# Optimization experiments

Measured on AMD Instinct MI355X. Metric: run time of the kernel, lower is better.

Reference implementation:

```python
import jax, jax.numpy as jnp
import numpy as np

N_NODES = 50000
N_EDGES = 800000
IN_DIM = 128
OUT_DIM = 64
K_KERNELS = 2
S_ATTEN = 2


def setup_inputs() -> dict:
    key = jax.random.key(0)
    ks = jax.random.split(key, 9)
    return {
        "x": jax.random.normal(ks[0], (N_NODES, IN_DIM), dtype=jnp.float32),
        "support_vals": jax.random.uniform(ks[1], (K_KERNELS, N_EDGES), dtype=jnp.float32),
        "atten_vals": jax.random.uniform(ks[2], (S_ATTEN, N_EDGES), dtype=jnp.float32),
        "W_transform": jax.random.normal(ks[3], (K_KERNELS, IN_DIM, OUT_DIM), dtype=jnp.float32) * 0.05,
        "w_left": jax.random.normal(ks[4], (K_KERNELS, S_ATTEN + 1, OUT_DIM), dtype=jnp.float32) * 0.05,
        "w_right": jax.random.normal(ks[5], (K_KERNELS, S_ATTEN + 1, OUT_DIM), dtype=jnp.float32) * 0.05,
        "W_residual": jax.random.normal(ks[6], (IN_DIM + OUT_DIM, OUT_DIM), dtype=jnp.float32) * 0.05,
        "edge_rows": jax.random.randint(ks[7], (N_EDGES,), 0, N_NODES, dtype=jnp.int64),
        "edge_cols": jax.random.randint(ks[8], (N_EDGES,), 0, N_NODES, dtype=jnp.int64),
    }


def reference(x, support_vals, atten_vals, W_transform, w_left, w_right, W_residual, edge_rows, edge_cols):
    # x: [N, F], edge lists: [E]; all supports share the same sparsity pattern.
    N = x.shape[0]
    K = W_transform.shape[0]
    output = jnp.zeros((N, W_transform.shape[2]), dtype=x.dtype)
    for k in range(K):
        wx = x @ W_transform[k]                       # [N, D]
        al = wx @ w_left[k].T                         # [N, S+1]
        ar = wx @ w_right[k].T                        # [N, S+1]
        # per-support edge values; support i=S uses this kernel's Cheb support
        vals = jnp.concatenate([atten_vals, support_vals[k][None, :]], axis=0)  # [S+1, E]
        # score_e = sum_i (al[row_e,i] + ar[col_e,i]) * vals[i,e]
        scores = jnp.einsum('es,se->e', al[edge_rows] + ar[edge_cols], vals)    # [E]
        # row-wise (segment) softmax over nonzeros, as tf.sparse_softmax
        m = jax.ops.segment_max(scores, edge_rows, num_segments=N)              # [N]
        ex = jnp.exp(scores - m[edge_rows])
        denom = jax.ops.segment_sum(ex, edge_rows, num_segments=N)              # [N]
        probs = ex / denom[edge_rows]                                           # [E]
        # spmm: out[r] = sum_{e: row_e=r} probs_e * wx[col_e]
        output = output + jax.ops.segment_sum(probs[:, None] * wx[edge_cols], edge_rows, num_segments=N)
    # residual projection then elu activation
    output = jnp.concatenate([x, output], axis=-1) @ W_residual
    return jax.nn.elu(output)
```

## Files before the change

### kernel.cpp

```cpp
#include <hip/hip_runtime.h>

#define N_NODES 50000
#define N_EDGES 800000
#define IN_DIM 128
#define OUT_DIM 64
#define NEG_INF (-1e30f)
#define GBLK ((N_NODES + 63) / 64)
#define BSHIFT 7
#define NBUK ((N_NODES + 127) >> 7)
#define NBUKP 392
#define EB 1024
#define PREB ((N_EDGES + EB - 1) / EB)
#define NFRAG (3 * 16 + 8)
#define STAGE_CAP 3072

typedef unsigned short ushort_t;
typedef __attribute__((ext_vector_type(8))) short short8;
typedef __attribute__((ext_vector_type(4))) float f32x4;

__device__ __forceinline__ unsigned f2bf(float f) {
    unsigned u = __float_as_uint(f);
    u += 0x7fffu + ((u >> 16) & 1u);
    return u >> 16;
}
__device__ __forceinline__ unsigned rl_u(unsigned v, int i) {
    return __builtin_amdgcn_readlane(v, i);
}
__device__ __forceinline__ float rl_f(float v, int i) {
    return __uint_as_float(__builtin_amdgcn_readlane(__float_as_uint(v), i));
}

__global__ void wpack_kernel(const float* __restrict__ Wt,
                             const float* __restrict__ Wres,
                             ushort_t* __restrict__ Wpack) {
    int idx = blockIdx.x * 256 + threadIdx.x;
    if (idx >= NFRAG * 512) return;
    int f = idx >> 9;
    int within = idx & 511;
    int lane = within >> 3;
    int b = within & 7;
    float val;
    if (f < 48) {
        int mat = f >> 4;
        int ct = (f >> 2) & 3;
        int kc = f & 3;
        int k = kc * 32 + (lane >> 4) * 8 + b;
        int c = ct * 16 + (lane & 15);
        const float* W = (mat < 2) ? (Wt + (size_t)mat * IN_DIM * OUT_DIM) : Wres;
        val = W[(size_t)k * OUT_DIM + c];
    } else {
        int f2 = f - 48;
        int ct = f2 >> 1;
        int kc = f2 & 1;
        int k = kc * 32 + (lane >> 4) * 8 + b;
        int c = ct * 16 + (lane & 15);
        val = Wres[(size_t)(IN_DIM + k) * OUT_DIM + c];
    }
    Wpack[idx] = (ushort_t)f2bf(val);
}

__global__ __launch_bounds__(256) void gemm_kernel(
        const float* __restrict__ x,
        const ushort_t* __restrict__ Wpack,
        const float* __restrict__ wl,
        const float* __restrict__ wr,
        unsigned* __restrict__ wxi,
        float* __restrict__ xres,
        float* __restrict__ al,
        float* __restrict__ ar) {
    int wave = threadIdx.x >> 6;
    int lane = threadIdx.x & 63;
    int lr = lane & 15;
    int lg = lane >> 4;
    int row0 = blockIdx.x * 64 + wave * 16;

    int arow = row0 + lr;
    if (arow >= N_NODES) arow = N_NODES - 1;
    const float* xr = x + (size_t)arow * IN_DIM;
    short8 afrag[4];
#pragma unroll
    for (int kc = 0; kc < 4; ++kc) {
        float4 f0 = *(const float4*)(xr + kc * 32 + lg * 8);
        float4 f1 = *(const float4*)(xr + kc * 32 + lg * 8 + 4);
        short8 a;
        a[0] = (short)f2bf(f0.x); a[1] = (short)f2bf(f0.y);
        a[2] = (short)f2bf(f0.z); a[3] = (short)f2bf(f0.w);
        a[4] = (short)f2bf(f1.x); a[5] = (short)f2bf(f1.y);
        a[6] = (short)f2bf(f1.z); a[7] = (short)f2bf(f1.w);
        afrag[kc] = a;
    }

    f32x4 acc[3][4] = {};
#pragma unroll
    for (int kc = 0; kc < 4; ++kc) {
#pragma unroll
        for (int mat = 0; mat < 3; ++mat) {
#pragma unroll
            for (int ct = 0; ct < 4; ++ct) {
                short8 bfrag = *(const short8*)(
                    Wpack + (size_t)(((mat * 4 + ct) * 4 + kc) << 9) + lane * 8);
                acc[mat][ct] = __builtin_amdgcn_mfma_f32_16x16x32_bf16(
                    afrag[kc], bfrag, acc[mat][ct], 0, 0, 0);
            }
        }
    }

#pragma unroll
    for (int r = 0; r < 4; ++r) {
        int gr = row0 + lg * 4 + r;
        if (gr < N_NODES) {
#pragma unroll
            for (int ct = 0; ct < 4; ++ct) {
                unsigned pk = f2bf(acc[0][ct][r]) | (f2bf(acc[1][ct][r]) << 16);
                wxi[(size_t)gr * OUT_DIM + ct * 16 + lr] = pk;
                xres[(size_t)gr * OUT_DIM + ct * 16 + lr] = acc[2][ct][r];
            }
        }
    }

#pragma unroll
    for (int mat = 0; mat < 2; ++mat) {
#pragma unroll
        for (int s = 0; s < 3; ++s) {
            float wlv[4], wrv[4];
#pragma unroll
            for (int ct = 0; ct < 4; ++ct) {
                wlv[ct] = wl[(size_t)(mat * 3 + s) * OUT_DIM + ct * 16 + lr];
                wrv[ct] = wr[(size_t)(mat * 3 + s) * OUT_DIM + ct * 16 + lr];
            }
#pragma unroll
            for (int r = 0; r < 4; ++r) {
                float pl = 0.f, pr = 0.f;
#pragma unroll
                for (int ct = 0; ct < 4; ++ct) {
                    pl = fmaf(acc[mat][ct][r], wlv[ct], pl);
                    pr = fmaf(acc[mat][ct][r], wrv[ct], pr);
                }
#pragma unroll
                for (int off = 1; off < 16; off <<= 1) {
                    pl += __shfl_xor(pl, off);
                    pr += __shfl_xor(pr, off);
                }
                if (lr == 0) {
                    int gr = row0 + lg * 4 + r;
                    if (gr < N_NODES) {
                        al[(size_t)gr * 6 + mat * 3 + s] = pl;
                        ar[(size_t)gr * 6 + mat * 3 + s] = pr;
                    }
                }
            }
        }
    }
}

__global__ __launch_bounds__(256) void score_sort_kernel(
        const int* __restrict__ rows,
        const int* __restrict__ cols,
        const float* __restrict__ atten,
        const float* __restrict__ support,
        const float* __restrict__ al,
        const float* __restrict__ ar,
        uint4* __restrict__ etmp,
        uint2* __restrict__ cl) {
    __shared__ int cnt[512];
    __shared__ int cur[512];
    __shared__ int aux[256];
    __shared__ uint4 stage[EB];
    int t = threadIdx.x;
    cnt[t] = 0; cnt[t + 256] = 0;
    __syncthreads();
    int base0 = blockIdx.x * EB;
    int nval = min(EB, N_EDGES - base0);

    int r_[4], c_[4];
    float s0_[4], s1_[4];
#pragma unroll
    for (int i = 0; i < 4; ++i) {
        int e = base0 + i * 256 + t;
        bool v = e < N_EDGES;
        int r = v ? rows[e] : -1;
        int c = v ? cols[e] : 0;
        float sc0 = 0.f, sc1 = 0.f;
        if (v) {
            float a0 = atten[e], a1 = atten[N_EDGES + e];
            float sp0 = support[e], sp1 = support[N_EDGES + e];
            const float* A = al + (size_t)r * 6;
            const float* B = ar + (size_t)c * 6;
            sc0 = (A[0] + B[0]) * a0 + (A[1] + B[1]) * a1 + (A[2] + B[2]) * sp0;
            sc1 = (A[3] + B[3]) * a0 + (A[4] + B[4]) * a1 + (A[5] + B[5]) * sp1;
            atomicAdd(&cnt[r >> BSHIFT], 1);
        }
        r_[i] = r; c_[i] = c; s0_[i] = sc0; s1_[i] = sc1;
    }
    __syncthreads();
    int a0 = cnt[2 * t], a1 = cnt[2 * t + 1];
    int ps = a0 + a1;
    aux[t] = ps;
    __syncthreads();
    int val = ps;
    for (int off = 1; off < 256; off <<= 1) {
        int y = (t >= off) ? aux[t - off] : 0;
        __syncthreads();
        val += y; aux[t] = val;
        __syncthreads();
    }
    int e2 = val - ps;
    cur[2 * t] = e2;
    cur[2 * t + 1] = e2 + a0;
    size_t cb = (size_t)blockIdx.x * NBUKP;
    if (2 * t < NBUK)     cl[cb + 2 * t]     = make_uint2((unsigned)a0, (unsigned)e2);
    if (2 * t + 1 < NBUK) cl[cb + 2 * t + 1] = make_uint2((unsigned)a1, (unsigned)(e2 + a0));
    __syncthreads();
#pragma unroll
    for (int i = 0; i < 4; ++i) {
        if (r_[i] < 0) continue;
        int pos = atomicAdd(&cur[r_[i] >> BSHIFT], 1);
        uint4 pv;
        pv.x = (unsigned)c_[i] | ((unsigned)(r_[i] & 127) << 16);
        pv.y = __float_as_uint(s0_[i]);
        pv.z = __float_as_uint(s1_[i]);
        pv.w = 0u;
        stage[pos] = pv;
    }
    __syncthreads();
    for (int i = t; i < nval; i += 256)
        etmp[(size_t)base0 + i] = stage[i];
}

__global__ void colscan_kernel(const uint2* __restrict__ cl,
                               int* __restrict__ btot) {
    __shared__ int sh[256];
    int k = blockIdx.x, t = threadIdx.x;
    int s = 0;
    for (int b = t; b < PREB; b += 256) s += (int)cl[(size_t)b * NBUKP + k].x;
    sh[t] = s;
    __syncthreads();
    for (int off = 128; off > 0; off >>= 1) {
        if (t < off) sh[t] += sh[t + off];
        __syncthreads();
    }
    if (t == 0) btot[k] = sh[0];
}

__global__ __launch_bounds__(256) void sortb_kernel(
        const uint2* __restrict__ cl,
        const int* __restrict__ btot,
        const uint4* __restrict__ etmp,
        uint4* __restrict__ edata,
        int* __restrict__ row_ptr) {
    __shared__ uint4 stage[STAGE_CAP];
    __shared__ int rpos[PREB + 2];
    __shared__ int lloff[PREB];
    __shared__ int aux[256];
    __shared__ int bb[512];
    __shared__ int hist[128], rcur[128];
    int k = blockIdx.x, t = threadIdx.x;

    bb[t] = (t < NBUK) ? btot[t] : 0;
    bb[t + 256] = (t + 256 < NBUK) ? btot[t + 256] : 0;
    __syncthreads();
    int a0 = bb[2 * t], a1 = bb[2 * t + 1];
    int ps = a0 + a1;
    aux[t] = ps;
    __syncthreads();
    int val = ps;
    for (int off = 1; off < 256; off <<= 1) {
        int y = (t >= off) ? aux[t - off] : 0;
        __syncthreads();
        val += y; aux[t] = val;
        __syncthreads();
    }
    bb[2 * t] = val - ps;
    bb[2 * t + 1] = val - ps + a0;
    __syncthreads();
    int base = bb[k];

    for (int b = t; b < PREB; b += 256) {
        uint2 v2 = cl[(size_t)b * NBUKP + k];
        rpos[b] = (int)v2.x;
        lloff[b] = (int)v2.y;
    }
    if (t < 128) hist[t] = 0;
    __syncthreads();
    int v[4];
    int idx4 = 4 * t;
#pragma unroll
    for (int i = 0; i < 4; ++i) v[i] = (idx4 + i < PREB) ? rpos[idx4 + i] : 0;
    __syncthreads();
    int s = 0;
#pragma unroll
    for (int i = 0; i < 4; ++i) { int tmp = v[i]; v[i] = s; s += tmp; }
    aux[t] = s;
    __syncthreads();
    int tv = s;
    for (int off = 1; off < 256; off <<= 1) {
        int y = (t >= off) ? aux[t - off] : 0;
        __syncthreads();
        tv += y; aux[t] = tv;
        __syncthreads();
    }
    int ofs = tv - s;
#pragma unroll
    for (int i = 0; i < 4; ++i)
        if (idx4 + i <= PREB) rpos[idx4 + i] = ofs + v[i];
    __syncthreads();
    int nb = rpos[PREB];

    for (int b = t; b < PREB; b += 256) {
        int s0 = rpos[b];
        int n = rpos[b + 1] - s0;
        int lo = lloff[b];
        const uint4* src = etmp + (size_t)b * EB + lo;
        for (int i = 0; i < n; ++i) {
            uint4 rec = src[i];
            int j = s0 + i;
            if (j < STAGE_CAP) stage[j] = rec;
            atomicAdd(&hist[(rec.x >> 16) & 127], 1);
        }
    }
    __syncthreads();
    int hv = (t < 128) ? hist[t] : 0;
    aux[t] = hv;
    __syncthreads();
    int hval = hv;
    for (int off = 1; off < 128; off <<= 1) {
        int y = (t >= off && t < 128) ? aux[t - off] : 0;
        __syncthreads();
        hval += y; aux[t] = hval;
        __syncthreads();
    }
    if (t < 128) {
        rcur[t] = hval - hv;
        int row = (k << BSHIFT) + t;
        if (row < N_NODES) row_ptr[row] = base + hval - hv;
    }
    if (k == NBUK - 1 && t == 0) row_ptr[N_NODES] = N_EDGES;
    __syncthreads();
    for (int j = t; j < nb; j += 256) {
        uint4 rec;
        if (j < STAGE_CAP) rec = stage[j];
        else {
            int lo = 0, hi = PREB - 1;
            while (lo < hi) { int mid = (lo + hi + 1) >> 1; if (rpos[mid] <= j) lo = mid; else hi = mid - 1; }
            rec = etmp[(size_t)lo * EB + lloff[lo] + (j - rpos[lo])];
        }
        int rl = (rec.x >> 16) & 127;
        int dst = atomicAdd(&rcur[rl], 1);
        edata[(size_t)base + dst] = rec;
    }
}

__global__ void attn_kernel(const int* __restrict__ row_ptr,
                            const uint4* __restrict__ edata,
                            const unsigned* __restrict__ wxi,
                            ushort_t* __restrict__ aacc) {
    int wid = blockIdx.x * 4 + (threadIdx.x >> 6);
    if (wid >= N_NODES) return;
    int lane = threadIdx.x & 63;
    int beg = row_ptr[wid], end = row_ptr[wid + 1];
    int deg = end - beg;
    float a = 0.f;

    if (deg > 0 && deg <= 64) {
        bool valid = lane < deg;
        uint4 ed = edata[valid ? beg + lane : beg];
        unsigned c = ed.x & 0xFFFFu;
        float sc0 = valid ? __uint_as_float(ed.y) : NEG_INF;
        float sc1 = valid ? __uint_as_float(ed.z) : NEG_INF;
        float m0 = sc0, m1 = sc1;
#pragma unroll
        for (int off = 32; off > 0; off >>= 1) {
            m0 = fmaxf(m0, __shfl_xor(m0, off));
            m1 = fmaxf(m1, __shfl_xor(m1, off));
        }
        float e0 = valid ? __expf(sc0 - m0) : 0.f;
        float e1 = valid ? __expf(sc1 - m1) : 0.f;
        float l0 = e0, l1 = e1;
#pragma unroll
        for (int off = 32; off > 0; off >>= 1) {
            l0 += __shfl_xor(l0, off);
            l1 += __shfl_xor(l1, off);
        }
        float p0 = e0 / l0;
        float p1 = e1 / l1;
        float acc8[8] = {};
        int i = 0;
        for (; i + 8 <= deg; i += 8) {
            unsigned cc[8], vv[8];
#pragma unroll
            for (int j = 0; j < 8; ++j) cc[j] = rl_u(c, i + j);
#pragma unroll
            for (int j = 0; j < 8; ++j) vv[j] = wxi[(size_t)cc[j] * OUT_DIM + lane];
#pragma unroll
            for (int j = 0; j < 8; ++j) {
                acc8[j] = fmaf(rl_f(p0, i + j), __uint_as_float(vv[j] << 16), acc8[j]);
                acc8[j] = fmaf(rl_f(p1, i + j), __uint_as_float(vv[j] & 0xffff0000u), acc8[j]);
            }
        }
        for (; i < deg; ++i) {
            unsigned ci = rl_u(c, i);
            unsigned v = wxi[(size_t)ci * OUT_DIM + lane];
            acc8[0] = fmaf(rl_f(p0, i), __uint_as_float(v << 16), acc8[0]);
            acc8[0] = fmaf(rl_f(p1, i), __uint_as_float(v & 0xffff0000u), acc8[0]);
        }
        a = ((acc8[0] + acc8[1]) + (acc8[2] + acc8[3]))
          + ((acc8[4] + acc8[5]) + (acc8[6] + acc8[7]));
    } else if (deg > 64) {
        float m0 = NEG_INF, l0 = 0.f, m1 = NEG_INF, l1 = 0.f;
        for (int base = beg; base < end; base += 64) {
            int pos = base + lane;
            bool valid = pos < end;
            uint4 ed = edata[valid ? pos : beg];
            float sc0 = valid ? __uint_as_float(ed.y) : NEG_INF;
            float sc1 = valid ? __uint_as_float(ed.z) : NEG_INF;
            float cm0 = sc0, cm1 = sc1;
#pragma unroll
            for (int off = 32; off > 0; off >>= 1) {
                cm0 = fmaxf(cm0, __shfl_xor(cm0, off));
                cm1 = fmaxf(cm1, __shfl_xor(cm1, off));
            }
            float mn0 = fmaxf(m0, cm0), mn1 = fmaxf(m1, cm1);
            float e0 = valid ? __expf(sc0 - mn0) : 0.f;
            float e1 = valid ? __expf(sc1 - mn1) : 0.f;
#pragma unroll
            for (int off = 32; off > 0; off >>= 1) {
                e0 += __shfl_xor(e0, off);
                e1 += __shfl_xor(e1, off);
            }
            l0 = l0 * __expf(m0 - mn0) + e0;
            l1 = l1 * __expf(m1 - mn1) + e1;
            m0 = mn0; m1 = mn1;
        }
        float inv0 = 1.f / l0, inv1 = 1.f / l1;
        for (int base = beg; base < end; base += 64) {
            int pos = base + lane;
            bool valid = pos < end;
            uint4 ed = edata[valid ? pos : beg];
            unsigned c = ed.x & 0xFFFFu;
            float p0 = valid ? __expf(__uint_as_float(ed.y) - m0) * inv0 : 0.f;
            float p1 = valid ? __expf(__uint_as_float(ed.z) - m1) * inv1 : 0.f;
            int cnt = min(64, end - base);
            for (int i = 0; i < cnt; ++i) {
                unsigned ci = rl_u(c, i);
                unsigned v = wxi[(size_t)ci * OUT_DIM + lane];
                a = fmaf(rl_f(p0, i), __uint_as_float(v << 16), a);
                a = fmaf(rl_f(p1, i), __uint_as_float(v & 0xffff0000u), a);
            }
        }
    }
    aacc[(size_t)wid * OUT_DIM + lane] = (ushort_t)f2bf(a);
}

__global__ __launch_bounds__(256) void resid_kernel(
        const ushort_t* __restrict__ aacc,
        const float* __restrict__ xres,
        const ushort_t* __restrict__ Wpack,
        float* __restrict__ out) {
    int wave = threadIdx.x >> 6;
    int lane = threadIdx.x & 63;
    int lr = lane & 15;
    int lg = lane >> 4;
    int row0 = blockIdx.x * 64 + wave * 16;
    int arow = row0 + lr;
    if (arow >= N_NODES) arow = N_NODES - 1;
    const ushort_t* ap = aacc + (size_t)arow * OUT_DIM;
    short8 af[2];
#pragma unroll
    for (int kc = 0; kc < 2; ++kc)
        af[kc] = *(const short8*)(ap + kc * 32 + lg * 8);
    f32x4 acc4[4] = {};
#pragma unroll
    for (int kc = 0; kc < 2; ++kc) {
#pragma unroll
        for (int ct = 0; ct < 4; ++ct) {
            short8 bfrag = *(const short8*)(
                Wpack + (size_t)((48 + ct * 2 + kc) << 9) + lane * 8);
            acc4[ct] = __builtin_amdgcn_mfma_f32_16x16x32_bf16(
                af[kc], bfrag, acc4[ct], 0, 0, 0);
        }
    }
#pragma unroll
    for (int r = 0; r < 4; ++r) {
        int gr = row0 + lg * 4 + r;
        if (gr < N_NODES) {
#pragma unroll
            for (int ct = 0; ct < 4; ++ct) {
                float v = acc4[ct][r] + xres[(size_t)gr * OUT_DIM + ct * 16 + lr];
                out[(size_t)gr * OUT_DIM + ct * 16 + lr] = (v > 0.f) ? v : expm1f(v);
            }
        }
    }
}

extern "C" void kernel_launch(void* const* d_in, const int* in_sizes, int n_in,
                              void* d_out, int out_size, void* d_ws, size_t ws_size,
                              hipStream_t stream) {
    const float* x       = (const float*)d_in[0];
    const float* support = (const float*)d_in[1];
    const float* atten   = (const float*)d_in[2];
    const float* Wt      = (const float*)d_in[3];
    const float* wl      = (const float*)d_in[4];
    const float* wr      = (const float*)d_in[5];
    const float* Wres    = (const float*)d_in[6];
    const int*   rows    = (const int*)d_in[7];
    const int*   cols    = (const int*)d_in[8];
    float* out = (float*)d_out;

    unsigned* wxi   = (unsigned*)d_ws;
    float* xres     = (float*)(wxi + (size_t)N_NODES * OUT_DIM);
    float* al       = xres + (size_t)N_NODES * OUT_DIM;
    float* ar       = al + (size_t)N_NODES * 6;
    uint4* etmp     = (uint4*)(ar + (size_t)N_NODES * 6);
    uint4* edata    = etmp + (size_t)N_EDGES;
    int*   row_ptr  = (int*)(edata + (size_t)N_EDGES);
    uint2* cl       = (uint2*)(row_ptr + N_NODES + 4);
    int*   btot     = (int*)(cl + (size_t)PREB * NBUKP);
    ushort_t* Wpack = (ushort_t*)(btot + NBUK + 4);
    ushort_t* aacc  = (ushort_t*)etmp;

    wpack_kernel<<<(NFRAG * 512 + 255) / 256, 256, 0, stream>>>(Wt, Wres, Wpack);
    gemm_kernel<<<GBLK, 256, 0, stream>>>(x, Wpack, wl, wr, wxi, xres, al, ar);
    score_sort_kernel<<<PREB, 256, 0, stream>>>(
        rows, cols, atten, support, al, ar, etmp, cl);
    colscan_kernel<<<NBUK, 256, 0, stream>>>(cl, btot);
    sortb_kernel<<<NBUK, 256, 0, stream>>>(
        cl, btot, etmp, edata, row_ptr);
    attn_kernel<<<(N_NODES + 3) / 4, 256, 0, stream>>>(
        row_ptr, edata, wxi, aacc);
    resid_kernel<<<GBLK, 256, 0, stream>>>(aacc, xres, Wpack, out);
}
```

Baseline: 140.3 us.

## Use fp16 dot2 for SpMM accumulation and fold bucket totals into score kernel

Two changes. First, wx for the two kernels is stored as packed fp16 pairs instead of bf16, and the edge probabilities are packed as half2, so each neighbour accumulates with a single v_dot2 instruction instead of two FMAs plus unpacking. Second, the separate column-scan kernel that summed per-bucket counts is removed; score_sort now atomically adds its counts into btot, which is cleared by a memset beforehand. The intent is to cut ALU work in the attention loop and one kernel launch, at the cost of fp16 range and precision limits and global atomic contention.

```diff
diff --git a/kernel.cpp b/kernel.cpp
--- a/kernel.cpp
+++ b/kernel.cpp
@@ -17,6 +17,7 @@
 typedef unsigned short ushort_t;
 typedef __attribute__((ext_vector_type(8))) short short8;
 typedef __attribute__((ext_vector_type(4))) float f32x4;
+typedef __attribute__((ext_vector_type(2))) _Float16 half2_t;
 
 __device__ __forceinline__ unsigned f2bf(float f) {
     unsigned u = __float_as_uint(f);
@@ -28,6 +29,15 @@
 }
 __device__ __forceinline__ float rl_f(float v, int i) {
     return __uint_as_float(__builtin_amdgcn_readlane(__float_as_uint(v), i));
+}
+__device__ __forceinline__ unsigned pack_h2(float a, float b) {
+    auto h = __builtin_amdgcn_cvt_pkrtz(a, b);
+    union { decltype(h) h2; unsigned u; } v; v.h2 = h; return v.u;
+}
+__device__ __forceinline__ float dot2u(unsigned w, unsigned p, float acc) {
+    union { unsigned u; half2_t h; } wv, pv;
+    wv.u = w; pv.u = p;
+    return __builtin_amdgcn_fdot2(wv.h, pv.h, acc, false);
 }
 
 __global__ void wpack_kernel(const float* __restrict__ Wt,
@@ -111,8 +121,8 @@
         if (gr < N_NODES) {
 #pragma unroll
             for (int ct = 0; ct < 4; ++ct) {
-                unsigned pk = f2bf(acc[0][ct][r]) | (f2bf(acc[1][ct][r]) << 16);
-                wxi[(size_t)gr * OUT_DIM + ct * 16 + lr] = pk;
+                wxi[(size_t)gr * OUT_DIM + ct * 16 + lr] =
+                    pack_h2(acc[0][ct][r], acc[1][ct][r]);
                 xres[(size_t)gr * OUT_DIM + ct * 16 + lr] = acc[2][ct][r];
             }
         }
@@ -161,7 +171,8 @@
         const float* __restrict__ al,
         const float* __restrict__ ar,
         uint4* __restrict__ etmp,
-        uint2* __restrict__ cl) {
+        uint2* __restrict__ cl,
+        int* __restrict__ btot) {
     __shared__ int cnt[512];
     __shared__ int cur[512];
     __shared__ int aux[256];
@@ -208,8 +219,14 @@
     cur[2 * t] = e2;
     cur[2 * t + 1] = e2 + a0;
     size_t cb = (size_t)blockIdx.x * NBUKP;
-    if (2 * t < NBUK)     cl[cb + 2 * t]     = make_uint2((unsigned)a0, (unsigned)e2);
-    if (2 * t + 1 < NBUK) cl[cb + 2 * t + 1] = make_uint2((unsigned)a1, (unsigned)(e2 + a0));
+    if (2 * t < NBUK) {
+        cl[cb + 2 * t] = make_uint2((unsigned)a0, (unsigned)e2);
+        if (a0) atomicAdd(&btot[2 * t], a0);
+    }
+    if (2 * t + 1 < NBUK) {
+        cl[cb + 2 * t + 1] = make_uint2((unsigned)a1, (unsigned)(e2 + a0));
+        if (a1) atomicAdd(&btot[2 * t + 1], a1);
+    }
     __syncthreads();
 #pragma unroll
     for (int i = 0; i < 4; ++i) {
@@ -225,21 +242,6 @@
     __syncthreads();
     for (int i = t; i < nval; i += 256)
         etmp[(size_t)base0 + i] = stage[i];
-}
-
-__global__ void colscan_kernel(const uint2* __restrict__ cl,
-                               int* __restrict__ btot) {
-    __shared__ int sh[256];
-    int k = blockIdx.x, t = threadIdx.x;
-    int s = 0;
-    for (int b = t; b < PREB; b += 256) s += (int)cl[(size_t)b * NBUKP + k].x;
-    sh[t] = s;
-    __syncthreads();
-    for (int off = 128; off > 0; off >>= 1) {
-        if (t < off) sh[t] += sh[t + off];
-        __syncthreads();
-    }
-    if (t == 0) btot[k] = sh[0];
 }
 
 __global__ __launch_bounds__(256) void sortb_kernel(
@@ -381,8 +383,7 @@
             l0 += __shfl_xor(l0, off);
             l1 += __shfl_xor(l1, off);
         }
-        float p0 = e0 / l0;
-        float p1 = e1 / l1;
+        unsigned pp = pack_h2(e0 / l0, e1 / l1);
         float acc8[8] = {};
         int i = 0;
         for (; i + 8 <= deg; i += 8) {
@@ -392,16 +393,13 @@
 #pragma unroll
             for (int j = 0; j < 8; ++j) vv[j] = wxi[(size_t)cc[j] * OUT_DIM + lane];
 #pragma unroll
-            for (int j = 0; j < 8; ++j) {
-                acc8[j] = fmaf(rl_f(p0, i + j), __uint_as_float(vv[j] << 16), acc8[j]);
-                acc8[j] = fmaf(rl_f(p1, i + j), __uint_as_float(vv[j] & 0xffff0000u), acc8[j]);
-            }
+            for (int j = 0; j < 8; ++j)
+                acc8[j] = dot2u(vv[j], rl_u(pp, i + j), acc8[j]);
         }
         for (; i < deg; ++i) {
             unsigned ci = rl_u(c, i);
             unsigned v = wxi[(size_t)ci * OUT_DIM + lane];
-            acc8[0] = fmaf(rl_f(p0, i), __uint_as_float(v << 16), acc8[0]);
-            acc8[0] = fmaf(rl_f(p1, i), __uint_as_float(v & 0xffff0000u), acc8[0]);
+            acc8[0] = dot2u(v, rl_u(pp, i), acc8[0]);
         }
         a = ((acc8[0] + acc8[1]) + (acc8[2] + acc8[3]))
           + ((acc8[4] + acc8[5]) + (acc8[6] + acc8[7]));
@@ -439,12 +437,12 @@
             unsigned c = ed.x & 0xFFFFu;
             float p0 = valid ? __expf(__uint_as_float(ed.y) - m0) * inv0 : 0.f;
             float p1 = valid ? __expf(__uint_as_float(ed.z) - m1) * inv1 : 0.f;
+            unsigned pp = pack_h2(p0, p1);
             int cnt = min(64, end - base);
             for (int i = 0; i < cnt; ++i) {
                 unsigned ci = rl_u(c, i);
                 unsigned v = wxi[(size_t)ci * OUT_DIM + lane];
-                a = fmaf(rl_f(p0, i), __uint_as_float(v << 16), a);
-                a = fmaf(rl_f(p1, i), __uint_as_float(v & 0xffff0000u), a);
+                a = dot2u(v, rl_u(pp, i), a);
             }
         }
     }
@@ -518,11 +516,12 @@
     ushort_t* Wpack = (ushort_t*)(btot + NBUK + 4);
     ushort_t* aacc  = (ushort_t*)etmp;
 
+    (void)hipMemsetAsync(btot, 0, NBUK * sizeof(int), stream);
+
     wpack_kernel<<<(NFRAG * 512 + 255) / 256, 256, 0, stream>>>(Wt, Wres, Wpack);
     gemm_kernel<<<GBLK, 256, 0, stream>>>(x, Wpack, wl, wr, wxi, xres, al, ar);
     score_sort_kernel<<<PREB, 256, 0, stream>>>(
-        rows, cols, atten, support, al, ar, etmp, cl);
-    colscan_kernel<<<NBUK, 256, 0, stream>>>(cl, btot);
+        rows, cols, atten, support, al, ar, etmp, cl, btot);
     sortb_kernel<<<NBUK, 256, 0, stream>>>(
         cl, btot, etmp, edata, row_ptr);
     attn_kernel<<<(N_NODES + 3) / 4, 256, 0, stream>>>(
```

After: 186.8 us. +33.2%, slower.
